# Performance work log

Measured on AMD Instinct MI355X. Metric: run time of the kernel, lower is better.

Reference implementation:

```python
import jax, jax.numpy as jnp
import numpy as np

B, S, D = 4, 2048, 1024
H, DH = 16, 64  # num_heads, output_dim per head
NEG = -1e9


def setup_inputs() -> dict:
    key = jax.random.key(0)
    ks = jax.random.split(key, 12)
    inp = {
        "query": jax.random.normal(ks[0], (B, S, D), dtype=jnp.float32),
        "key": jax.random.normal(ks[1], (B, S, D), dtype=jnp.float32),
        "value": jax.random.normal(ks[2], (B, S, D), dtype=jnp.float32),
        "mask": jax.random.randint(ks[3], (B, S, S), 0, 2, dtype=jnp.int32),
    }
    sc = 1.0 / np.sqrt(D)
    sco = 1.0 / np.sqrt(H * DH)
    # stacked per-head projection weights: [H, D, DH] (nn.Linear applies x @ W.T; we store W.T directly)
    inp["Wq"] = jax.random.uniform(ks[4], (H, D, DH), jnp.float32, -sc, sc)
    inp["bq"] = jax.random.uniform(ks[5], (H, DH), jnp.float32, -sc, sc)
    inp["Wk"] = jax.random.uniform(ks[6], (H, D, DH), jnp.float32, -sc, sc)
    inp["bk"] = jax.random.uniform(ks[7], (H, DH), jnp.float32, -sc, sc)
    inp["Wv"] = jax.random.uniform(ks[8], (H, D, DH), jnp.float32, -sc, sc)
    inp["bv"] = jax.random.uniform(ks[9], (H, DH), jnp.float32, -sc, sc)
    inp["Wo"] = jax.random.uniform(ks[10], (H * DH, DH), jnp.float32, -sco, sco)
    inp["bo"] = jax.random.uniform(ks[11], (DH,), jnp.float32, -sco, sco)
    return inp


def reference(query, key, value, mask, Wq, bq, Wk, bk, Wv, bv, Wo, bo):
    # batched per-head projections: [B,S,D] x [H,D,DH] -> [B,H,S,DH]
    q = jnp.einsum("bsd,hde->bhse", query, Wq) + bq[None, :, None, :]
    k = jnp.einsum("bsd,hde->bhse", key, Wk) + bk[None, :, None, :]
    v = jnp.einsum("bsd,hde->bhse", value, Wv) + bv[None, :, None, :]
    # NOTE: original module does NOT scale by 1/sqrt(DH)
    scores = jnp.einsum("bhse,bhte->bhst", q, k)  # [B,H,S,S]
    scores = jnp.where(mask[:, None, :, :] == 0, NEG, scores)
    attn = jax.nn.softmax(scores, axis=-1)
    out = jnp.einsum("bhst,bhte->bhse", attn, v)  # [B,H,S,DH]
    # concat heads (head order matches torch.cat over loop): [B,S,H*DH]
    cat = out.transpose(0, 2, 1, 3).reshape(query.shape[0], query.shape[1], -1)
    return cat @ Wo + bo
```

## Files before the change

### kernel.cpp

```cpp
#include <hip/hip_runtime.h>
#include <hip/hip_bf16.h>

typedef __attribute__((ext_vector_type(8))) short bf16x8;
typedef __attribute__((ext_vector_type(4))) float f32x4;
typedef unsigned int u32;
typedef unsigned short u16;
typedef unsigned long long u64;

typedef short s16x4 __attribute__((ext_vector_type(4)));
typedef s16x4 __attribute__((may_alias)) s16x4_ma;
typedef bf16x8 __attribute__((may_alias)) bf16x8_ma;
typedef u32 u32x4 __attribute__((ext_vector_type(4)));
typedef u32x4 __attribute__((may_alias)) u32x4_ma;


__device__ __forceinline__ void gload_lds16(const void* g, void* l) {
    __builtin_amdgcn_global_load_lds(
        (const __attribute__((address_space(1))) void*)g,
        (__attribute__((address_space(3))) void*)l, 16, 0, 0);
}

__device__ __forceinline__ u16 f2bf(float f) {
    u32 u = __builtin_bit_cast(u32, f);
    u32 r = u + 0x7fffu + ((u >> 16) & 1u);
    return (u16)(r >> 16);
}

__device__ __forceinline__ u32 pk2(float lo, float hi) {
    u32 a = __builtin_bit_cast(u32, lo) + 0x8000u;
    u32 b = __builtin_bit_cast(u32, hi) + 0x8000u;
    return __builtin_amdgcn_perm(b, a, 0x07060302u);
}

__global__ void k_pack_w(const float* __restrict__ W, u16* __restrict__ Wt) {
    int i = blockIdx.x * 256 + threadIdx.x;
    int h = i >> 16;
    int r = i & 65535;
    int k = r >> 6, e = r & 63;
    Wt[(size_t)(h * 64 + e) * 1024 + k] = f2bf(W[i]);
}

__global__ void k_pack_wo(const float* __restrict__ W, u16* __restrict__ Wt) {
    int i = blockIdx.x * 256 + threadIdx.x;
    int k = i >> 6, e = i & 63;
    Wt[(size_t)e * 1024 + k] = f2bf(W[i]);
}

__global__ void k_pack_mask(const int* __restrict__ mask, u32* __restrict__ bits) {
    size_t i = (size_t)blockIdx.x * 256 + threadIdx.x;
    int m = mask[i];
    u64 bal = __ballot(m != 0);
    if ((threadIdx.x & 63) == 0) *(u64*)(bits + (i >> 5)) = bal;
}

__global__ __launch_bounds__(256) void k_proj(
    const float* __restrict__ A, const u16* __restrict__ Bt,
    const float* __restrict__ bias, u16* __restrict__ out, int mode, float oscale)
{
    __shared__ char smem[16384];
    const int tid = threadIdx.x, lane = tid & 63, w = tid >> 6;
    const int wr = w >> 1, wc = w & 1;
    const int fr = lane & 15, fq = lane >> 4;

    const int flat = blockIdx.y * 8 + blockIdx.x;
    const int xcd = flat & 7, idx = flat >> 3;
    const int xb = idx >> 3;
    const int yb = xcd * 8 + (idx & 7);
    const int m0 = yb * 128, n0 = xb * 128;

    const int arow = w * 32 + (lane >> 2);
    const int aseg = (lane & 3) * 8;

    f32x4 acc[4][4] = {};

    for (int kt = 0; kt < 1024; kt += 32) {
#pragma unroll
        for (int t = 0; t < 2; ++t) {
            const float* src = A + (size_t)(m0 + arow + t * 16) * 1024 + kt + aseg;
            float4 v0 = *(const float4*)src;
            float4 v1 = *(const float4*)(src + 4);
            u32x4 pk = { pk2(v0.x, v0.y), pk2(v0.z, v0.w),
                         pk2(v1.x, v1.y), pk2(v1.z, v1.w) };
            *(u32x4_ma*)(smem + w * 2048 + t * 1024 + lane * 16) = pk;
            gload_lds16(Bt + (size_t)(n0 + arow + t * 16) * 1024 + kt + aseg,
                        smem + 8192 + w * 2048 + t * 1024);
        }
        __syncthreads();
        bf16x8 af[4], bfv[4];
#pragma unroll
        for (int m = 0; m < 4; ++m)
            af[m] = *(const bf16x8_ma*)(smem + (wr * 64 + m * 16 + fr) * 64 + fq * 16);
#pragma unroll
        for (int n = 0; n < 4; ++n)
            bfv[n] = *(const bf16x8_ma*)(smem + 8192 + (wc * 64 + n * 16 + fr) * 64 + fq * 16);
#pragma unroll
        for (int m = 0; m < 4; ++m)
#pragma unroll
            for (int n = 0; n < 4; ++n)
                acc[m][n] = __builtin_amdgcn_mfma_f32_16x16x32_bf16(af[m], bfv[n], acc[m][n], 0, 0, 0);
        __syncthreads();
    }

#pragma unroll
    for (int m = 0; m < 4; ++m) {
#pragma unroll
        for (int n = 0; n < 4; ++n) {
            int col = n0 + wc * 64 + n * 16 + fr;
            float bvv = bias[col];
            int h = col >> 6, e = col & 63;
            if (mode == 0) {
#pragma unroll
                for (int j = 0; j < 4; ++j) {
                    int row = m0 + wr * 64 + m * 16 + fq * 4 + j;
                    int bb = row >> 11, s = row & 2047;
                    out[((size_t)(bb * 16 + h) * 2048 + s) * 64 + e] = f2bf((acc[m][n][j] + bvv) * oscale);
                }
            } else {
                int row = m0 + wr * 64 + m * 16 + fq * 4;
                int bb = row >> 11, s = row & 2047;
                ushort4 o = make_ushort4(f2bf(acc[m][n][0] + bvv), f2bf(acc[m][n][1] + bvv),
                                         f2bf(acc[m][n][2] + bvv), f2bf(acc[m][n][3] + bvv));
                *(ushort4*)(out + ((size_t)(bb * 16 + h) * 64 + e) * 2048 + s) = o;
            }
        }
    }
}

__global__ __launch_bounds__(512, 2) void k_attn(
    const u16* __restrict__ Qg_, const u16* __restrict__ Kg_,
    const u16* __restrict__ Vg_, const u32* __restrict__ mbits,
    u16* __restrict__ O)
{
    __shared__ char smem[81920];
    const int tid = threadIdx.x, lane = tid & 63, w = tid >> 6;
    const int fr = lane & 15, fq = lane >> 4;
    char* Ps = smem + 49152 + w * 4096;

    const int bid = blockIdx.x;
    const int wg = (bid & 7) * 64 + (bid >> 3);
    const int bh = wg >> 3, qt = wg & 7;
    const int b = bh >> 4;
    const int qw = qt * 256 + w * 32;

    const u16* Qg = Qg_ + (size_t)bh * 2048 * 64;
    const u16* Kg = Kg_ + (size_t)bh * 2048 * 64;
    const u16* Vg = Vg_ + (size_t)bh * 64 * 2048;

    bf16x8 qf[2][2];
#pragma unroll
    for (int m = 0; m < 2; ++m)
#pragma unroll
        for (int ks = 0; ks < 2; ++ks)
            qf[m][ks] = *(const bf16x8_ma*)(Qg + (size_t)(qw + m * 16 + fr) * 64 + ks * 32 + fq * 8);

    f32x4 acc[2][4] = {};
    f32x4 acc_l[2] = {};

    const bf16x8 onesv = {(short)0x3F80, (short)0x3F80, (short)0x3F80, (short)0x3F80,
                          (short)0x3F80, (short)0x3F80, (short)0x3F80, (short)0x3F80};

    const int srow = w * 8 + (lane >> 3);
    const int sseg = (lane & 7) ^ (srow & 7);

    gload_lds16(Kg + (size_t)srow * 64 + sseg * 8, smem + w * 1024);
    gload_lds16(Vg + (size_t)srow * 2048 + sseg * 8, smem + 8192 + w * 1024);
    gload_lds16(Kg + (size_t)(64 + srow) * 64 + sseg * 8, smem + 16384 + w * 1024);
    gload_lds16(Vg + (size_t)srow * 2048 + 64 + sseg * 8, smem + 16384 + 8192 + w * 1024);
    asm volatile("s_waitcnt vmcnt(2)" ::: "memory");
    __builtin_amdgcn_s_barrier();

    const u32* mp = mbits + ((size_t)b * 2048 + qw + fr) * 64;

    int rb = 0;
    for (int t = 0; t < 32; ++t) {
        char* Ks = smem + rb * 16384;
        char* Vs = Ks + 8192;

        u64 mwv[2];
        mwv[0] = *(const u64*)(mp + t * 2);
        mwv[1] = *(const u64*)(mp + 1024 + t * 2);
        __builtin_amdgcn_sched_barrier(0);

        if (t + 2 < 32) {
            int wb = rb == 0 ? 2 : rb - 1;
            char* Kn = smem + wb * 16384;
            int kvn = (t + 2) * 64;
            gload_lds16(Kg + (size_t)(kvn + srow) * 64 + sseg * 8, Kn + w * 1024);
            gload_lds16(Vg + (size_t)srow * 2048 + kvn + sseg * 8, Kn + 8192 + w * 1024);
        }

        f32x4 sc[4][2] = {};
        __builtin_amdgcn_s_setprio(1);
#pragma unroll
        for (int ks = 0; ks < 2; ++ks) {
#pragma unroll
            for (int n = 0; n < 4; ++n) {
                int row = n * 16 + fr;
                bf16x8 kf = *(const bf16x8_ma*)(Ks + row * 128 + (((ks * 4 + fq) ^ (row & 7)) << 4));
#pragma unroll
                for (int m = 0; m < 2; ++m)
                    sc[n][m] = __builtin_amdgcn_mfma_f32_16x16x32_bf16(kf, qf[m][ks], sc[n][m], 0, 0, 0);
            }
        }
        __builtin_amdgcn_s_setprio(0);

#pragma unroll
        for (int m = 0; m < 2; ++m) {
            const int ql = m * 16 + fr;
            u32 lo = (u32)mwv[m], hi = (u32)(mwv[m] >> 32);
#pragma unroll
            for (int n = 0; n < 4; ++n) {
                u32 word = (n & 2) ? hi : lo;
                int sh = ((n & 1) << 4) + fq * 4;
                float p0 = __builtin_amdgcn_exp2f(((word >> sh) & 1) ? sc[n][m][0] : -128.f);
                float p1 = __builtin_amdgcn_exp2f(((word >> (sh + 1)) & 1) ? sc[n][m][1] : -128.f);
                float p2 = __builtin_amdgcn_exp2f(((word >> (sh + 2)) & 1) ? sc[n][m][2] : -128.f);
                float p3 = __builtin_amdgcn_exp2f(((word >> (sh + 3)) & 1) ? sc[n][m][3] : -128.f);
                u32 pa = pk2(p0, p1);
                u32 pb = pk2(p2, p3);
                u64 v = (u64)pa | ((u64)pb << 32);
                int seg = (n * 2 + (fq >> 1)) ^ (ql & 7);
                *(s16x4_ma*)(Ps + ql * 128 + seg * 16 + (fq & 1) * 8) =
                    __builtin_bit_cast(s16x4, v);
            }
        }
        asm volatile("" ::: "memory");

        __builtin_amdgcn_s_setprio(1);
#pragma unroll
        for (int ks = 0; ks < 2; ++ks) {
            bf16x8 pf[2];
#pragma unroll
            for (int m = 0; m < 2; ++m) {
                int row = m * 16 + fr;
                pf[m] = *(const bf16x8_ma*)(Ps + row * 128 + (((ks * 4 + fq) ^ (row & 7)) << 4));
            }
#pragma unroll
            for (int m = 0; m < 2; ++m)
                acc_l[m] = __builtin_amdgcn_mfma_f32_16x16x32_bf16(pf[m], onesv, acc_l[m], 0, 0, 0);
#pragma unroll
            for (int ne = 0; ne < 4; ++ne) {
                int vrow = ne * 16 + fr;
                bf16x8 vf = *(const bf16x8_ma*)(Vs + vrow * 128 + (((ks * 4 + fq) ^ (vrow & 7)) << 4));
#pragma unroll
                for (int m = 0; m < 2; ++m)
                    acc[m][ne] = __builtin_amdgcn_mfma_f32_16x16x32_bf16(pf[m], vf, acc[m][ne], 0, 0, 0);
            }
        }
        __builtin_amdgcn_s_setprio(0);

        asm volatile("s_waitcnt vmcnt(2)" ::: "memory");
        __builtin_amdgcn_s_barrier();
        rb = rb == 2 ? 0 : rb + 1;
    }

    const int h = bh & 15;
#pragma unroll
    for (int m = 0; m < 2; ++m)
#pragma unroll
        for (int j = 0; j < 4; ++j) {
            float inv = 1.0f / acc_l[m][j];
            int sq = qw + m * 16 + fq * 4 + j;
#pragma unroll
            for (int ne = 0; ne < 4; ++ne)
                O[((size_t)b * 2048 + sq) * 1024 + h * 64 + ne * 16 + fr] =
                    f2bf(acc[m][ne][j] * inv);
        }
}

__global__ __launch_bounds__(256) void k_oproj(
    const u16* __restrict__ A, const u16* __restrict__ Bt,
    const float* __restrict__ bo, float* __restrict__ out)
{
    __shared__ char smem[8192 + 4096];
    const int tid = threadIdx.x, lane = tid & 63, w = tid >> 6;
    const int fr = lane & 15, fq = lane >> 4;
    const int m0 = blockIdx.x * 128;

    const int arow = w * 32 + (lane >> 2);
    const int aseg = (lane & 3) * 8;
    const int brow = w * 16 + (lane >> 2);

    f32x4 acc[2][4] = {};

    for (int kt = 0; kt < 1024; kt += 32) {
#pragma unroll
        for (int t = 0; t < 2; ++t)
            gload_lds16(A + (size_t)(m0 + arow + t * 16) * 1024 + kt + aseg,
                        smem + w * 2048 + t * 1024);
        gload_lds16(Bt + (size_t)brow * 1024 + kt + aseg, smem + 8192 + w * 1024);
        __syncthreads();
        bf16x8 af[2], bfv[4];
#pragma unroll
        for (int m = 0; m < 2; ++m)
            af[m] = *(const bf16x8_ma*)(smem + (w * 32 + m * 16 + fr) * 64 + fq * 16);
#pragma unroll
        for (int n = 0; n < 4; ++n)
            bfv[n] = *(const bf16x8_ma*)(smem + 8192 + (n * 16 + fr) * 64 + fq * 16);
#pragma unroll
        for (int m = 0; m < 2; ++m)
#pragma unroll
            for (int n = 0; n < 4; ++n)
                acc[m][n] = __builtin_amdgcn_mfma_f32_16x16x32_bf16(af[m], bfv[n], acc[m][n], 0, 0, 0);
        __syncthreads();
    }

#pragma unroll
    for (int m = 0; m < 2; ++m)
#pragma unroll
        for (int n = 0; n < 4; ++n) {
            float bb = bo[n * 16 + fr];
#pragma unroll
            for (int j = 0; j < 4; ++j)
                out[(size_t)(m0 + w * 32 + m * 16 + fq * 4 + j) * 64 + n * 16 + fr] =
                    acc[m][n][j] + bb;
        }
}

extern "C" void kernel_launch(void* const* d_in, const int* in_sizes, int n_in,
                              void* d_out, int out_size, void* d_ws, size_t ws_size,
                              hipStream_t stream) {
    const float* query = (const float*)d_in[0];
    const float* key   = (const float*)d_in[1];
    const float* value = (const float*)d_in[2];
    const int*   mask  = (const int*)d_in[3];
    const float* Wq = (const float*)d_in[4];
    const float* bq = (const float*)d_in[5];
    const float* Wk = (const float*)d_in[6];
    const float* bk = (const float*)d_in[7];
    const float* Wv = (const float*)d_in[8];
    const float* bv = (const float*)d_in[9];
    const float* Wo = (const float*)d_in[10];
    const float* bo = (const float*)d_in[11];
    float* out = (float*)d_out;

    char* ws = (char*)d_ws;
    size_t off = 0;
    auto alloc = [&](size_t bytes) {
        size_t o = off;
        off += (bytes + 255) & ~(size_t)255;
        return o;
    };
    u16* attno = (u16*)(ws + alloc(16777216));
    u16* wtq = (u16*)(ws + alloc(2097152));
    u16* wtk = (u16*)(ws + alloc(2097152));
    u16* wtv = (u16*)(ws + alloc(2097152));
    u16* wot = (u16*)(ws + alloc(131072));
    u16* qh  = (u16*)(ws + alloc(16777216));
    u16* kh  = (u16*)(ws + alloc(16777216));
    u16* vt  = (u16*)(ws + alloc(16777216));
    u32* mb  = (u32*)(ws + alloc(2097152));

    k_pack_w<<<4096, 256, 0, stream>>>(Wq, wtq);
    k_pack_w<<<4096, 256, 0, stream>>>(Wk, wtk);
    k_pack_w<<<4096, 256, 0, stream>>>(Wv, wtv);
    k_pack_wo<<<256, 256, 0, stream>>>(Wo, wot);
    k_pack_mask<<<65536, 256, 0, stream>>>(mask, mb);

    k_proj<<<dim3(8, 64), 256, 0, stream>>>(query, wtq, bq, qh, 0, 1.44269504088896f);
    k_proj<<<dim3(8, 64), 256, 0, stream>>>(key,   wtk, bk, kh, 0, 1.0f);
    k_proj<<<dim3(8, 64), 256, 0, stream>>>(value, wtv, bv, vt, 1, 1.0f);

    k_attn<<<512, 512, 0, stream>>>(qh, kh, vt, mb, attno);

    k_oproj<<<64, 256, 0, stream>>>(attno, wot, bo, out);
}
```

Before: 340.8 us.

## Double-buffer K-loop loads in projection and output-projection GEMMs

The k_proj and k_oproj loops now prefetch the next K-slice while the current one is being multiplied. The weight tile uses double-buffered LDS via global_load_lds, and in k_proj the fp32 activations are held in registers. Barriers are replaced with explicit s_waitcnt vmcnt counts plus raw s_barrier, so the loads for the next tile stay in flight during the MFMAs. The cost is more LDS and registers, and correctness now depends on the hand-written vmcnt counts matching the number of outstanding loads.

```diff
diff --git a/kernel.cpp b/kernel.cpp
--- a/kernel.cpp
+++ b/kernel.cpp
@@ -57,7 +57,7 @@
     const float* __restrict__ A, const u16* __restrict__ Bt,
     const float* __restrict__ bias, u16* __restrict__ out, int mode, float oscale)
 {
-    __shared__ char smem[16384];
+    __shared__ char smem[24576];
     const int tid = threadIdx.x, lane = tid & 63, w = tid >> 6;
     const int wr = w >> 1, wc = w & 1;
     const int fr = lane & 15, fq = lane >> 4;
@@ -72,33 +72,58 @@
     const int aseg = (lane & 3) * 8;
 
     f32x4 acc[4][4] = {};
+    float4 cur[2][2], nxt[2][2];
+
+#pragma unroll
+    for (int t = 0; t < 2; ++t)
+        gload_lds16(Bt + (size_t)(n0 + arow + t * 16) * 1024 + aseg,
+                    smem + 8192 + w * 2048 + t * 1024);
+#pragma unroll
+    for (int t = 0; t < 2; ++t) {
+        const float* src = A + (size_t)(m0 + arow + t * 16) * 1024 + aseg;
+        cur[t][0] = *(const float4*)src;
+        cur[t][1] = *(const float4*)(src + 4);
+    }
 
     for (int kt = 0; kt < 1024; kt += 32) {
+        const int bb = (kt >> 5) & 1;
+        if (kt + 32 < 1024) {
+#pragma unroll
+            for (int t = 0; t < 2; ++t)
+                gload_lds16(Bt + (size_t)(n0 + arow + t * 16) * 1024 + kt + 32 + aseg,
+                            smem + 8192 + (bb ^ 1) * 8192 + w * 2048 + t * 1024);
+#pragma unroll
+            for (int t = 0; t < 2; ++t) {
+                const float* src = A + (size_t)(m0 + arow + t * 16) * 1024 + kt + 32 + aseg;
+                nxt[t][0] = *(const float4*)src;
+                nxt[t][1] = *(const float4*)(src + 4);
+            }
+        }
 #pragma unroll
         for (int t = 0; t < 2; ++t) {
-            const float* src = A + (size_t)(m0 + arow + t * 16) * 1024 + kt + aseg;
-            float4 v0 = *(const float4*)src;
-            float4 v1 = *(const float4*)(src + 4);
-            u32x4 pk = { pk2(v0.x, v0.y), pk2(v0.z, v0.w),
-                         pk2(v1.x, v1.y), pk2(v1.z, v1.w) };
+            u32x4 pk = { pk2(cur[t][0].x, cur[t][0].y), pk2(cur[t][0].z, cur[t][0].w),
+                         pk2(cur[t][1].x, cur[t][1].y), pk2(cur[t][1].z, cur[t][1].w) };
             *(u32x4_ma*)(smem + w * 2048 + t * 1024 + lane * 16) = pk;
-            gload_lds16(Bt + (size_t)(n0 + arow + t * 16) * 1024 + kt + aseg,
-                        smem + 8192 + w * 2048 + t * 1024);
-        }
-        __syncthreads();
+        }
+        asm volatile("s_waitcnt vmcnt(6) lgkmcnt(0)" ::: "memory");
+        __builtin_amdgcn_sched_barrier(0);
+        __builtin_amdgcn_s_barrier();
+
         bf16x8 af[4], bfv[4];
 #pragma unroll
         for (int m = 0; m < 4; ++m)
             af[m] = *(const bf16x8_ma*)(smem + (wr * 64 + m * 16 + fr) * 64 + fq * 16);
 #pragma unroll
         for (int n = 0; n < 4; ++n)
-            bfv[n] = *(const bf16x8_ma*)(smem + 8192 + (wc * 64 + n * 16 + fr) * 64 + fq * 16);
+            bfv[n] = *(const bf16x8_ma*)(smem + 8192 + bb * 8192 + (wc * 64 + n * 16 + fr) * 64 + fq * 16);
 #pragma unroll
         for (int m = 0; m < 4; ++m)
 #pragma unroll
             for (int n = 0; n < 4; ++n)
                 acc[m][n] = __builtin_amdgcn_mfma_f32_16x16x32_bf16(af[m], bfv[n], acc[m][n], 0, 0, 0);
-        __syncthreads();
+        __builtin_amdgcn_s_barrier();
+#pragma unroll
+        for (int t = 0; t < 2; ++t) { cur[t][0] = nxt[t][0]; cur[t][1] = nxt[t][1]; }
     }
 
 #pragma unroll
@@ -112,15 +137,15 @@
 #pragma unroll
                 for (int j = 0; j < 4; ++j) {
                     int row = m0 + wr * 64 + m * 16 + fq * 4 + j;
-                    int bb = row >> 11, s = row & 2047;
-                    out[((size_t)(bb * 16 + h) * 2048 + s) * 64 + e] = f2bf((acc[m][n][j] + bvv) * oscale);
+                    int bb2 = row >> 11, s = row & 2047;
+                    out[((size_t)(bb2 * 16 + h) * 2048 + s) * 64 + e] = f2bf((acc[m][n][j] + bvv) * oscale);
                 }
             } else {
                 int row = m0 + wr * 64 + m * 16 + fq * 4;
-                int bb = row >> 11, s = row & 2047;
+                int bb2 = row >> 11, s = row & 2047;
                 ushort4 o = make_ushort4(f2bf(acc[m][n][0] + bvv), f2bf(acc[m][n][1] + bvv),
                                          f2bf(acc[m][n][2] + bvv), f2bf(acc[m][n][3] + bvv));
-                *(ushort4*)(out + ((size_t)(bb * 16 + h) * 64 + e) * 2048 + s) = o;
+                *(ushort4*)(out + ((size_t)(bb2 * 16 + h) * 64 + e) * 2048 + s) = o;
             }
         }
     }
@@ -272,7 +297,7 @@
     const u16* __restrict__ A, const u16* __restrict__ Bt,
     const float* __restrict__ bo, float* __restrict__ out)
 {
-    __shared__ char smem[8192 + 4096];
+    __shared__ char smem[24576];
     const int tid = threadIdx.x, lane = tid & 63, w = tid >> 6;
     const int fr = lane & 15, fq = lane >> 4;
     const int m0 = blockIdx.x * 128;
@@ -283,26 +308,41 @@
 
     f32x4 acc[2][4] = {};
 
+#pragma unroll
+    for (int t = 0; t < 2; ++t)
+        gload_lds16(A + (size_t)(m0 + arow + t * 16) * 1024 + aseg,
+                    smem + w * 2048 + t * 1024);
+    gload_lds16(Bt + (size_t)brow * 1024 + aseg, smem + 16384 + w * 1024);
+
     for (int kt = 0; kt < 1024; kt += 32) {
-#pragma unroll
-        for (int t = 0; t < 2; ++t)
-            gload_lds16(A + (size_t)(m0 + arow + t * 16) * 1024 + kt + aseg,
-                        smem + w * 2048 + t * 1024);
-        gload_lds16(Bt + (size_t)brow * 1024 + kt + aseg, smem + 8192 + w * 1024);
-        __syncthreads();
+        const int bb = (kt >> 5) & 1;
+        if (kt + 32 < 1024) {
+#pragma unroll
+            for (int t = 0; t < 2; ++t)
+                gload_lds16(A + (size_t)(m0 + arow + t * 16) * 1024 + kt + 32 + aseg,
+                            smem + (bb ^ 1) * 8192 + w * 2048 + t * 1024);
+            gload_lds16(Bt + (size_t)brow * 1024 + kt + 32 + aseg,
+                        smem + 16384 + (bb ^ 1) * 4096 + w * 1024);
+            asm volatile("s_waitcnt vmcnt(3)" ::: "memory");
+        } else {
+            asm volatile("s_waitcnt vmcnt(0)" ::: "memory");
+        }
+        __builtin_amdgcn_sched_barrier(0);
+        __builtin_amdgcn_s_barrier();
+
         bf16x8 af[2], bfv[4];
 #pragma unroll
         for (int m = 0; m < 2; ++m)
-            af[m] = *(const bf16x8_ma*)(smem + (w * 32 + m * 16 + fr) * 64 + fq * 16);
+            af[m] = *(const bf16x8_ma*)(smem + bb * 8192 + (w * 32 + m * 16 + fr) * 64 + fq * 16);
 #pragma unroll
         for (int n = 0; n < 4; ++n)
-            bfv[n] = *(const bf16x8_ma*)(smem + 8192 + (n * 16 + fr) * 64 + fq * 16);
+            bfv[n] = *(const bf16x8_ma*)(smem + 16384 + bb * 4096 + (n * 16 + fr) * 64 + fq * 16);
 #pragma unroll
         for (int m = 0; m < 2; ++m)
 #pragma unroll
             for (int n = 0; n < 4; ++n)
                 acc[m][n] = __builtin_amdgcn_mfma_f32_16x16x32_bf16(af[m], bfv[n], acc[m][n], 0, 0, 0);
-        __syncthreads();
+        __builtin_amdgcn_s_barrier();
     }
 
 #pragma unroll
```

New measurement: 332.3 us. 2.5% less time.
